# Optimization experiments

Measured on AMD Instinct MI355X. Metric: run time of the kernel, lower is better.

Reference implementation:

```python
import jax, jax.numpy as jnp
import numpy as np

RES = 0.1


def setup_inputs() -> dict:
    key = jax.random.key(0)
    k1, k2 = jax.random.split(key)
    B, N, H, W = 512, 8192, 200, 200
    # positions in [-11, 11] so some points land out of the valid [-9.9, 9.9] range
    opState = jax.random.uniform(k1, (B, N, 2), dtype=jnp.float32, minval=-11.0, maxval=11.0)
    # ESDF distances in [0, 2) meters
    envs = jax.random.uniform(k2, (B, 1, H, W), dtype=jnp.float32) * 2.0
    return {"opState": opState, "envs": envs}


def reference(opState, envs):
    # opState: [B, N, 2] world positions; envs: [B, 1, 200, 200] ESDF map
    out_range = jnp.any((opState < -9.9) | (opState > 9.9), axis=-1)  # [B, N]
    pos = jnp.clip(opState, -9.9, 9.9)
    pos_m = pos - 0.5 * RES
    idx = jnp.floor((pos_m + 10.0) / RES).astype(jnp.int32)           # [B, N, 2]
    idx_pos = (idx.astype(jnp.float32) + 0.5) * RES - 10.0
    diff = (pos - idx_pos) / RES                                       # [B, N, 2]

    esdf = envs[:, 0]                                                  # [B, H, W]
    b = jnp.arange(esdf.shape[0])[:, None]                             # [B, 1]
    ix, iy = idx[..., 0], idx[..., 1]
    # 4-corner gather for bilinear interpolation
    v00 = esdf[b, ix,     iy    ]
    v10 = esdf[b, ix + 1, iy    ]
    v01 = esdf[b, ix,     iy + 1]
    v11 = esdf[b, ix + 1, iy + 1]

    dx, dy = diff[..., 0], diff[..., 1]
    vx0 = (1.0 - dx) * v00 + dx * v10
    vx1 = (1.0 - dx) * v01 + dx * v11
    v = (1.0 - dy) * vx0 + dy * vx1
    dists = jnp.where(out_range, -1.0, v)                              # [B, N]

    viod = 10.0 * (0.3 - dists)
    penalty = jnp.square(jax.nn.relu(viod))  # positiveSmoothedL2
    return jnp.mean(penalty)
```

## Files before the change

### kernel.cpp

```cpp
#include <hip/hip_runtime.h>

#define RES 0.1f

constexpr int B_ = 512;
constexpr int N_ = 8192;
constexpr int H_ = 200;
constexpr int W_ = 200;
constexpr int MAP = H_ * W_;
constexpr long long TOTAL = (long long)B_ * N_;

constexpr int TPB = 1024;
constexpr int PPT = 8;
constexpr int V4  = PPT / 2;

__global__ __launch_bounds__(TPB) void collision_lds(
    const float* __restrict__ opState,
    const float* __restrict__ envs,
    float* __restrict__ partial)
{
    __shared__ float smap[MAP];
    const int b   = blockIdx.x;
    const int tid = threadIdx.x;

    const float4* pts4 = (const float4*)((const float2*)opState + (long long)b * N_);
    float4 p[V4];
    #pragma unroll
    for (int k = 0; k < V4; ++k)
        p[k] = pts4[tid + k * TPB];

    {
        const float4* m4 = (const float4*)(envs + (long long)b * MAP);
        float4* s4 = (float4*)smap;
        #pragma unroll
        for (int j = 0; j < 10; ++j) {
            int idx = tid + j * TPB;
            if (idx < MAP / 4) s4[idx] = m4[idx];
        }
    }
    __syncthreads();

    float acc = 0.0f;
    #pragma unroll
    for (int k = 0; k < V4; ++k) {
        #pragma unroll
        for (int h = 0; h < 2; ++h) {
            const float qx = h ? p[k].z : p[k].x;
            const float qy = h ? p[k].w : p[k].y;

            bool out_range = (qx < -9.9f) | (qx > 9.9f) |
                             (qy < -9.9f) | (qy > 9.9f);

            float px = fminf(fmaxf(qx, -9.9f), 9.9f);
            float py = fminf(fmaxf(qy, -9.9f), 9.9f);

            float pmx = px - 0.5f * RES;
            float pmy = py - 0.5f * RES;

            int ix = (int)floorf((pmx + 10.0f) * 10.0f);
            int iy = (int)floorf((pmy + 10.0f) * 10.0f);

            float ipx = ((float)ix + 0.5f) * RES - 10.0f;
            float ipy = ((float)iy + 0.5f) * RES - 10.0f;

            float dx = (px - ipx) * 10.0f;
            float dy = (py - ipy) * 10.0f;

            int base = ix * W_ + iy;
            float v00 = smap[base];
            float v01 = smap[base + 1];
            float v10 = smap[base + W_];
            float v11 = smap[base + W_ + 1];

            float vx0 = (1.0f - dx) * v00 + dx * v10;
            float vx1 = (1.0f - dx) * v01 + dx * v11;
            float v   = (1.0f - dy) * vx0 + dy * vx1;

            float dists = out_range ? -1.0f : v;
            float viod  = 10.0f * (0.3f - dists);
            float r     = viod > 0.0f ? viod : 0.0f;
            acc += r * r;
        }
    }

    #pragma unroll
    for (int off = 32; off > 0; off >>= 1)
        acc += __shfl_down(acc, off, 64);

    __shared__ float sacc[TPB / 64];
    const int lane = tid & 63;
    const int wid  = tid >> 6;
    if (lane == 0) sacc[wid] = acc;
    __syncthreads();

    if (tid == 0) {
        float s = 0.0f;
        #pragma unroll
        for (int w = 0; w < TPB / 64; ++w) s += sacc[w];
        partial[b] = s;
    }
}

__global__ __launch_bounds__(512) void collision_final(
    const float* __restrict__ partial,
    float* __restrict__ out)
{
    float acc = partial[threadIdx.x];

    #pragma unroll
    for (int off = 32; off > 0; off >>= 1)
        acc += __shfl_down(acc, off, 64);

    __shared__ float sacc[8];
    const int lane = threadIdx.x & 63;
    const int wid  = threadIdx.x >> 6;
    if (lane == 0) sacc[wid] = acc;
    __syncthreads();

    if (threadIdx.x == 0) {
        float s = 0.0f;
        #pragma unroll
        for (int w = 0; w < 8; ++w) s += sacc[w];
        out[0] = s / (float)TOTAL;
    }
}

extern "C" void kernel_launch(void* const* d_in, const int* in_sizes, int n_in,
                              void* d_out, int out_size, void* d_ws, size_t ws_size,
                              hipStream_t stream) {
    const float* opState = (const float*)d_in[0];
    const float* envs    = (const float*)d_in[1];
    float* out     = (float*)d_out;
    float* partial = (float*)d_ws;

    collision_lds<<<B_, TPB, 0, stream>>>(opState, envs, partial);
    collision_final<<<1, 512, 0, stream>>>(partial, out);
}
```

Baseline: 150.4 us.

## Replace LDS map staging with direct global gathers and XCD-aware block swizzle

Instead of copying each 160 KB ESDF map into shared memory per batch, each batch is split across four 256-thread blocks that gather the four bilinear corners directly from global memory. Block IDs are swizzled so that the sub-blocks of one batch share an XCD's L2, and loads are grouped to expose memory-level parallelism. This avoids reading whole maps when only sampled cells are needed, and it drops the LDS occupancy limit. The risk is many scattered cache-line requests whose cost depends on L2 hit rates.

```diff
diff --git a/kernel.cpp b/kernel.cpp
--- a/kernel.cpp
+++ b/kernel.cpp
@@ -9,46 +9,43 @@
 constexpr int MAP = H_ * W_;
 constexpr long long TOTAL = (long long)B_ * N_;
 
-constexpr int TPB = 1024;
-constexpr int PPT = 8;
-constexpr int V4  = PPT / 2;
+constexpr int TPB  = 256;
+constexpr int PPT  = 8;
+constexpr int SUBS = 4;
+constexpr int NBLK = B_ * SUBS;
+constexpr int GRP  = 4;
 
-__global__ __launch_bounds__(TPB) void collision_lds(
+__global__ __launch_bounds__(TPB) void collision_gather(
     const float* __restrict__ opState,
     const float* __restrict__ envs,
     float* __restrict__ partial)
 {
-    __shared__ float smap[MAP];
-    const int b   = blockIdx.x;
+    const int bid = blockIdx.x;
+    const int x    = bid & 7;
+    const int s    = bid >> 3;
+    const int batch = x * (B_ / 8) + (s >> 2);
+    const int sub   = s & 3;
+
     const int tid = threadIdx.x;
-
-    const float4* pts4 = (const float4*)((const float2*)opState + (long long)b * N_);
-    float4 p[V4];
-    #pragma unroll
-    for (int k = 0; k < V4; ++k)
-        p[k] = pts4[tid + k * TPB];
-
-    {
-        const float4* m4 = (const float4*)(envs + (long long)b * MAP);
-        float4* s4 = (float4*)smap;
-        #pragma unroll
-        for (int j = 0; j < 10; ++j) {
-            int idx = tid + j * TPB;
-            if (idx < MAP / 4) s4[idx] = m4[idx];
-        }
-    }
-    __syncthreads();
+    const float2* pts = (const float2*)opState + (long long)batch * N_ + sub * (N_ / SUBS);
+    const float*  m   = envs + (long long)batch * MAP;
 
     float acc = 0.0f;
+
     #pragma unroll
-    for (int k = 0; k < V4; ++k) {
+    for (int g = 0; g < PPT / GRP; ++g) {
+        float2 p[GRP];
         #pragma unroll
-        for (int h = 0; h < 2; ++h) {
-            const float qx = h ? p[k].z : p[k].x;
-            const float qy = h ? p[k].w : p[k].y;
+        for (int j = 0; j < GRP; ++j)
+            p[j] = pts[tid + (g * GRP + j) * TPB];
 
-            bool out_range = (qx < -9.9f) | (qx > 9.9f) |
-                             (qy < -9.9f) | (qy > 9.9f);
+        int   base[GRP];
+        float dxA[GRP], dyA[GRP];
+        bool  orA[GRP];
+        #pragma unroll
+        for (int j = 0; j < GRP; ++j) {
+            const float qx = p[j].x, qy = p[j].y;
+            orA[j] = (qx < -9.9f) | (qx > 9.9f) | (qy < -9.9f) | (qy > 9.9f);
 
             float px = fminf(fmaxf(qx, -9.9f), 9.9f);
             float py = fminf(fmaxf(qy, -9.9f), 9.9f);
@@ -62,20 +59,28 @@
             float ipx = ((float)ix + 0.5f) * RES - 10.0f;
             float ipy = ((float)iy + 0.5f) * RES - 10.0f;
 
-            float dx = (px - ipx) * 10.0f;
-            float dy = (py - ipy) * 10.0f;
+            dxA[j] = (px - ipx) * 10.0f;
+            dyA[j] = (py - ipy) * 10.0f;
+            base[j] = ix * W_ + iy;
+        }
 
-            int base = ix * W_ + iy;
-            float v00 = smap[base];
-            float v01 = smap[base + 1];
-            float v10 = smap[base + W_];
-            float v11 = smap[base + W_ + 1];
+        float v00[GRP], v01[GRP], v10[GRP], v11[GRP];
+        #pragma unroll
+        for (int j = 0; j < GRP; ++j) {
+            v00[j] = m[base[j]];
+            v01[j] = m[base[j] + 1];
+            v10[j] = m[base[j] + W_];
+            v11[j] = m[base[j] + W_ + 1];
+        }
 
-            float vx0 = (1.0f - dx) * v00 + dx * v10;
-            float vx1 = (1.0f - dx) * v01 + dx * v11;
+        #pragma unroll
+        for (int j = 0; j < GRP; ++j) {
+            float dx = dxA[j], dy = dyA[j];
+            float vx0 = (1.0f - dx) * v00[j] + dx * v10[j];
+            float vx1 = (1.0f - dx) * v01[j] + dx * v11[j];
             float v   = (1.0f - dy) * vx0 + dy * vx1;
 
-            float dists = out_range ? -1.0f : v;
+            float dists = orA[j] ? -1.0f : v;
             float viod  = 10.0f * (0.3f - dists);
             float r     = viod > 0.0f ? viod : 0.0f;
             acc += r * r;
@@ -93,33 +98,34 @@
     __syncthreads();
 
     if (tid == 0) {
-        float s = 0.0f;
+        float s2 = 0.0f;
         #pragma unroll
-        for (int w = 0; w < TPB / 64; ++w) s += sacc[w];
-        partial[b] = s;
+        for (int w = 0; w < TPB / 64; ++w) s2 += sacc[w];
+        partial[bid] = s2;
     }
 }
 
-__global__ __launch_bounds__(512) void collision_final(
+__global__ __launch_bounds__(256) void collision_final(
     const float* __restrict__ partial,
     float* __restrict__ out)
 {
-    float acc = partial[threadIdx.x];
+    float acc = 0.0f;
+    #pragma unroll
+    for (int k = 0; k < NBLK / 256; ++k)
+        acc += partial[threadIdx.x + k * 256];
 
     #pragma unroll
     for (int off = 32; off > 0; off >>= 1)
         acc += __shfl_down(acc, off, 64);
 
-    __shared__ float sacc[8];
+    __shared__ float sacc[4];
     const int lane = threadIdx.x & 63;
     const int wid  = threadIdx.x >> 6;
     if (lane == 0) sacc[wid] = acc;
     __syncthreads();
 
     if (threadIdx.x == 0) {
-        float s = 0.0f;
-        #pragma unroll
-        for (int w = 0; w < 8; ++w) s += sacc[w];
+        float s = sacc[0] + sacc[1] + sacc[2] + sacc[3];
         out[0] = s / (float)TOTAL;
     }
 }
@@ -132,6 +138,6 @@
     float* out     = (float*)d_out;
     float* partial = (float*)d_ws;
 
-    collision_lds<<<B_, TPB, 0, stream>>>(opState, envs, partial);
-    collision_final<<<1, 512, 0, stream>>>(partial, out);
+    collision_gather<<<NBLK, TPB, 0, stream>>>(opState, envs, partial);
+    collision_final<<<1, 256, 0, stream>>>(partial, out);
 }
```

Measured after the change: 171.1 us. 13.7% more time.
